# Kernel tuning notes

Measured on AMD Instinct MI355X. Metric: run time of the kernel, lower is better.

The kernel has to match this reference:

```python
import jax, jax.numpy as jnp
import numpy as np

I, H, O = 256, 512, 256  # input_size, hidden_size, output_size
B, S = 4096, 50


def _lstm_cell(x_t, h, c, Wih, Whh, bih, bhh):
    # torch gate order: i, f, g, o
    gates = x_t @ Wih.T + h @ Whh.T + bih + bhh  # [B, 4H]
    i, f, g, o = jnp.split(gates, 4, axis=-1)
    i = jax.nn.sigmoid(i)
    f = jax.nn.sigmoid(f)
    g = jnp.tanh(g)
    o = jax.nn.sigmoid(o)
    c_new = f * c + i * g
    h_new = o * jnp.tanh(c_new)
    return h_new, c_new


def setup_inputs() -> dict:
    key = jax.random.key(0)
    ks = jax.random.split(key, 12)
    s_i = 1.0 / np.sqrt(H)  # torch LSTM/Linear init scale
    u = lambda k, shape: jax.random.uniform(k, shape, jnp.float32, -s_i, s_i)
    return {
        "x": jax.random.normal(ks[0], (B, S, I), jnp.float32),
        "enc_Wih": u(ks[1], (4 * H, I)),
        "enc_Whh": u(ks[2], (4 * H, H)),
        "enc_bih": u(ks[3], (4 * H,)),
        "enc_bhh": u(ks[4], (4 * H,)),
        "dec_Wih": u(ks[5], (4 * H, I)),
        "dec_Whh": u(ks[6], (4 * H, H)),
        "dec_bih": u(ks[7], (4 * H,)),
        "dec_bhh": u(ks[8], (4 * H,)),
        "fc_W": u(ks[9], (O, H)),
        "fc_b": u(ks[10], (O,)),
        "target_seq_length": 20,
    }


def reference(x, enc_Wih, enc_Whh, enc_bih, enc_bhh,
              dec_Wih, dec_Whh, dec_bih, dec_bhh,
              fc_W, fc_b, target_seq_length):
    batch = x.shape[0]
    h0 = jnp.zeros((batch, H), x.dtype)
    c0 = jnp.zeros((batch, H), x.dtype)

    # ---- encoder: scan over time ----
    def enc_step(carry, x_t):
        h, c = carry
        h, c = _lstm_cell(x_t, h, c, enc_Wih, enc_Whh, enc_bih, enc_bhh)
        return (h, c), None

    (h, c), _ = jax.lax.scan(enc_step, (h0, c0), jnp.swapaxes(x, 0, 1))

    dec_in0 = jnp.zeros((batch, I), x.dtype)

    def dec_step(carry, _):
        h, c, inp = carry
        h, c = _lstm_cell(inp, h, c, dec_Wih, dec_Whh, dec_bih, dec_bhh)
        out = h @ fc_W.T + fc_b  # [B, O]
        return (h, c, out), out

    _, outs = jax.lax.scan(dec_step, (h, c, dec_in0), None,
                           length=target_seq_length)
    return jnp.swapaxes(outs, 0, 1)  # [B, T, O]
```

## Files before the change

kernel.cpp:

```cpp
#include <hip/hip_runtime.h>

#define I_SZ 256
#define H_SZ 512
#define O_SZ 256
#define B_SZ 4096
#define S_SZ 50
#define T_SZ 20
#define G4H  2048
#define BH   ((size_t)B_SZ * H_SZ)
#define NB   512
#define NSTEP (S_SZ + T_SZ)

#define PAD 72

typedef _Float16 half8 __attribute__((ext_vector_type(8)));
typedef float f32x4 __attribute__((ext_vector_type(4)));

__device__ __forceinline__ float sigm(float x) {
    return 1.0f / (1.0f + __expf(-x));
}
__device__ __forceinline__ float tanh_fast(float x) {
    float e = __expf(2.0f * x);
    return 1.0f - 2.0f / (e + 1.0f);
}

#define GLDS(gp, lp, aux) __builtin_amdgcn_global_load_lds(                 \
    (const __attribute__((address_space(1))) void*)(gp),                    \
    (__attribute__((address_space(3))) void*)(lp), 16, 0, (aux))

__global__ void k_zeroN(unsigned* p, int n) {
    int i = blockIdx.x * blockDim.x + threadIdx.x;
    if (i < n) p[i] = 0u;
}

__global__ void k_cvt(const float* __restrict__ src, _Float16* __restrict__ dst, int n) {
    int i = blockIdx.x * blockDim.x + threadIdx.x;
    if (i < n) dst[i] = (_Float16)src[i];
}

__global__ void k_bias_combine(const float* __restrict__ a, const float* __restrict__ b,
                               float* __restrict__ dst, int n) {
    int i = blockIdx.x * blockDim.x + threadIdx.x;
    if (i < n) dst[i] = a[i] + b[i];
}

__global__ __launch_bounds__(256) void k_cvt_x(const float* __restrict__ x,
                                               _Float16* __restrict__ xT) {
    size_t idx = ((size_t)blockIdx.x * 256 + threadIdx.x) * 8;
    int i = (int)(idx & 255);
    int s = (int)((idx >> 8) % S_SZ);
    size_t b = idx / (256 * S_SZ);
    float4 v0 = *(const float4*)(x + idx);
    float4 v1 = *(const float4*)(x + idx + 4);
    half8 hv;
    hv[0] = (_Float16)v0.x; hv[1] = (_Float16)v0.y;
    hv[2] = (_Float16)v0.z; hv[3] = (_Float16)v0.w;
    hv[4] = (_Float16)v1.x; hv[5] = (_Float16)v1.y;
    hv[6] = (_Float16)v1.z; hv[7] = (_Float16)v1.w;
    *(half8*)(xT + (((size_t)s * B_SZ + b) * I_SZ + i)) = hv;
}

__global__ void k_wenc(const float* __restrict__ eWih, const float* __restrict__ eWhh,
                       _Float16* __restrict__ Wenc) {
    int idx = blockIdx.x * blockDim.x + threadIdx.x;
    int r = idx / 768, col = idx % 768;
    float v = (col < 256) ? eWih[(size_t)r * 256 + col] : eWhh[(size_t)r * 512 + col - 256];
    Wenc[idx] = (_Float16)v;
}

__global__ __launch_bounds__(256) void k_wd(
    const float* __restrict__ dWhh, const float* __restrict__ dWih,
    const float* __restrict__ fcW, _Float16* __restrict__ Wd)
{
    __shared__ float sA[8][256];
    const int tid = threadIdx.x;
    const int r0 = blockIdx.x * 8;
    {
        int linear = tid * 8;
        int row = linear >> 8, col = linear & 255;
        const float4* p = (const float4*)(dWih + (size_t)(r0 + row) * 256 + col);
        float4 v0 = p[0], v1 = p[1];
        *(float4*)&sA[row][col]     = v0;
        *(float4*)&sA[row][col + 4] = v1;
    }
    __syncthreads();
    float acc[8][2] = {};
    const int k = tid;
    for (int i = 0; i < 256; ++i) {
        float w0 = fcW[(size_t)i * 512 + k];
        float w1 = fcW[(size_t)i * 512 + k + 256];
        #pragma unroll
        for (int rr = 0; rr < 8; ++rr) {
            float a = sA[rr][i];
            acc[rr][0] += a * w0;
            acc[rr][1] += a * w1;
        }
    }
    #pragma unroll
    for (int rr = 0; rr < 8; ++rr) {
        size_t base = (size_t)(r0 + rr) * 512;
        Wd[base + k]       = (_Float16)(dWhh[base + k]       + acc[rr][0]);
        Wd[base + k + 256] = (_Float16)(dWhh[base + k + 256] + acc[rr][1]);
    }
}

__global__ __launch_bounds__(256) void k_bd(
    const float* __restrict__ dWih, const float* __restrict__ fcb,
    const float* __restrict__ db, float* __restrict__ bd)
{
    __shared__ float sf[256];
    const int tid = threadIdx.x;
    sf[tid] = fcb[tid];
    __syncthreads();
    int r = blockIdx.x * 256 + tid;
    float acc = db[r];
    const float* row = dWih + (size_t)r * 256;
    for (int o = 0; o < 256; o += 4) {
        float4 v = *(const float4*)(row + o);
        acc += v.x * sf[o] + v.y * sf[o + 1] + v.z * sf[o + 2] + v.w * sf[o + 3];
    }
    bd[r] = acc;
}

__global__ __launch_bounds__(256, 2) void k_lstm_all(
    const _Float16* __restrict__ xT,
    const _Float16* __restrict__ Wenc,
    const _Float16* __restrict__ dWhh_h,
    const _Float16* __restrict__ Wd,
    const float* __restrict__ eb, const float* __restrict__ db,
    const float* __restrict__ bd,
    _Float16* __restrict__ h0buf, _Float16* __restrict__ h1buf,
    _Float16* __restrict__ hseq,
    unsigned* __restrict__ bar)
{
    __shared__ _Float16 lds[2][2][128 * 64];

    const int tid = threadIdx.x;
    const int xcd = blockIdx.x & 7, slot = blockIdx.x >> 3;
    const int mb = xcd * 4 + (slot >> 4);
    const int jb = slot & 15;
    const int m0 = mb * 128, j0 = jb * 32;
    unsigned* grp = bar + mb * 16;

    const int wv = tid >> 6, lane = tid & 63, lrow = lane & 15, lk8 = (lane >> 4) * 8;
    const int wm = wv >> 1, wn = wv & 1;

    const int colb  = (lane & 7) * 16;
    const int scolh = (colb ^ (((lane >> 3) & 7) << 4)) >> 1;
    int rowq[4], growq[4];
    #pragma unroll
    for (int q = 0; q < 4; ++q) {
        int r = q * 32 + wv * 8 + (lane >> 3);
        rowq[q] = r;
        growq[q] = ((r >> 4) & 3) * H_SZ + j0 + (r >> 6) * 16 + (r & 15);
    }

    float ebj[4], dbj[4], bdj[4];
    #pragma unroll
    for (int nf = 0; nf < 4; ++nf) {
        int col = nf * H_SZ + j0 + wn * 16 + lrow;
        ebj[nf] = eb[col]; dbj[nf] = db[col]; bdj[nf] = bd[col];
    }

    float creg[4][4];

    for (int step = 0; step < NSTEP; ++step) {
        const _Float16* xsrc; const _Float16* hin; const _Float16* W;
        _Float16* hout; int wstride, nx, niter;
        if (step < S_SZ) {
            xsrc = xT + (size_t)step * B_SZ * I_SZ;
            W = Wenc; wstride = 768; nx = 4;
            niter = (step == 0) ? 4 : 12;
            hin  = (step == 0) ? nullptr : ((step & 1) ? h0buf : h1buf);
            hout = (step == S_SZ - 1) ? hseq : ((step & 1) ? h1buf : h0buf);
        } else {
            int t = step - S_SZ;
            xsrc = nullptr; nx = 0; niter = 8; wstride = 512;
            W = (t == 0) ? dWhh_h : Wd;
            hin  = hseq + (size_t)t * BH;
            hout = hseq + (size_t)(t + 1) * BH;
        }

        auto wait_group = [&]() {
            if (tid == 0) {
                unsigned target = (unsigned)step * 16u;
                while (__hip_atomic_load(grp, __ATOMIC_RELAXED, __HIP_MEMORY_SCOPE_AGENT) < target)
                    __builtin_amdgcn_s_sleep(1);
            }
            __syncthreads();
        };

        auto stage = [&](int buf, int it) {
            const int koffW = it * 64;
            #pragma unroll
            for (int q = 0; q < 4; ++q) {
                const _Float16* gb = W + (size_t)growq[q] * wstride + koffW + scolh;
                GLDS(gb, &lds[buf][1][(q * 256 + wv * 64) * 8], 0);
            }
            if (it < nx) {
                #pragma unroll
                for (int q = 0; q < 4; ++q) {
                    const _Float16* ga = xsrc + (size_t)(m0 + rowq[q]) * I_SZ + it * 64 + scolh;
                    GLDS(ga, &lds[buf][0][(q * 256 + wv * 64) * 8], 0);
                }
            } else {
                #pragma unroll
                for (int q = 0; q < 4; ++q) {
                    const _Float16* ga = hin + (size_t)(m0 + rowq[q]) * H_SZ + (it - nx) * 64 + scolh;
                    GLDS(ga, &lds[buf][0][(q * 256 + wv * 64) * 8], 17);
                }
            }
        };

        f32x4 acc[4][4];
        #pragma unroll
        for (int mf = 0; mf < 4; ++mf)
            #pragma unroll
            for (int nf = 0; nf < 4; ++nf) {
                f32x4 z = {0.f, 0.f, 0.f, 0.f};
                acc[mf][nf] = z;
            }

        auto compute = [&](int buf) {
            #pragma unroll
            for (int kc = 0; kc < 2; ++kc) {
                const int cb = (kc * 32 + lk8) * 2;
                const int sc = (cb ^ ((lrow & 7) << 4)) >> 1;
                half8 a[4], b[4];
                #pragma unroll
                for (int mf = 0; mf < 4; ++mf)
                    a[mf] = *(const half8*)&lds[buf][0][(wm * 64 + mf * 16 + lrow) * 64 + sc];
                #pragma unroll
                for (int nf = 0; nf < 4; ++nf)
                    b[nf] = *(const half8*)&lds[buf][1][(wn * 64 + nf * 16 + lrow) * 64 + sc];
                #pragma unroll
                for (int mf = 0; mf < 4; ++mf)
                    #pragma unroll
                    for (int nf = 0; nf < 4; ++nf)
                        acc[mf][nf] = __builtin_amdgcn_mfma_f32_16x16x32_f16(a[mf], b[nf], acc[mf][nf], 0, 0, 0);
            }
        };

        if (step > 0 && nx == 0) wait_group();
        stage(0, 0);
        __syncthreads();
        int buf = 0;
        for (int it = 0; it < niter; ++it) {
            if (it + 1 < niter) {
                if (step > 0 && it + 1 == nx) wait_group();
                stage(buf ^ 1, it + 1);
            }
            compute(buf);
            __syncthreads();
            buf ^= 1;
        }

        float bj[4];
        #pragma unroll
        for (int nf = 0; nf < 4; ++nf)
            bj[nf] = (step < S_SZ) ? ebj[nf] : ((step == S_SZ) ? dbj[nf] : bdj[nf]);

        _Float16* hsm = &lds[0][0][0];
        const int lc = wn * 16 + lrow;
        #pragma unroll
        for (int mf = 0; mf < 4; ++mf)
            #pragma unroll
            for (int r = 0; r < 4; ++r) {
                int lr = wm * 64 + mf * 16 + (lane >> 4) * 4 + r;
                float gi = acc[mf][0][r] + bj[0];
                float gf = acc[mf][1][r] + bj[1];
                float gg = acc[mf][2][r] + bj[2];
                float go = acc[mf][3][r] + bj[3];
                float cold = (step == 0) ? 0.0f : creg[mf][r];
                float cn = sigm(gf) * cold + sigm(gi) * tanh_fast(gg);
                creg[mf][r] = cn;
                hsm[lr * 32 + lc] = (_Float16)(sigm(go) * tanh_fast(cn));
            }
        __syncthreads();
        {
            int row = tid >> 1, seg = tid & 1;
            const unsigned long long* src =
                (const unsigned long long*)&hsm[row * 32 + seg * 16];
            unsigned long long v0 = src[0], v1 = src[1], v2 = src[2], v3 = src[3];
            unsigned long long* dst =
                (unsigned long long*)(hout + (size_t)(m0 + row) * H_SZ + j0 + seg * 16);
            __hip_atomic_store(dst + 0, v0, __ATOMIC_RELAXED, __HIP_MEMORY_SCOPE_AGENT);
            __hip_atomic_store(dst + 1, v1, __ATOMIC_RELAXED, __HIP_MEMORY_SCOPE_AGENT);
            __hip_atomic_store(dst + 2, v2, __ATOMIC_RELAXED, __HIP_MEMORY_SCOPE_AGENT);
            __hip_atomic_store(dst + 3, v3, __ATOMIC_RELAXED, __HIP_MEMORY_SCOPE_AGENT);
        }

        if (step != NSTEP - 1) {
            __syncthreads();
            if (tid == 0)
                __hip_atomic_fetch_add(grp, 1u, __ATOMIC_RELAXED, __HIP_MEMORY_SCOPE_AGENT);
        }
    }
}

__global__ __launch_bounds__(256) void k_fc(
    const _Float16* __restrict__ hseq1,
    const _Float16* __restrict__ W,
    const float* __restrict__ bias,
    float* __restrict__ out)
{
    __shared__ _Float16 Asm[128][PAD];
    __shared__ _Float16 Bsm[128][PAD];

    const int tid = threadIdx.x;
    const int m0 = blockIdx.x * 128;
    const int t  = blockIdx.y;
    const int n0 = blockIdx.z * 128;
    const int wv = tid >> 6, lane = tid & 63, lrow = lane & 15, lk = (lane >> 4) * 8;
    const int wm = wv >> 1, wn = wv & 1;

    f32x4 acc[4][4] = {};

    const int srow = tid >> 3, skc = (tid & 7) * 8;
    const _Float16* A = hseq1 + (size_t)t * BH;

    for (int k0 = 0; k0 < H_SZ; k0 += 64) {
        __syncthreads();
        #pragma unroll
        for (int q = 0; q < 4; ++q) {
            int r = srow + q * 32;
            *(half8*)&Asm[r][skc] = *(const half8*)(A + (size_t)(m0 + r) * H_SZ + k0 + skc);
        }
        #pragma unroll
        for (int q = 0; q < 4; ++q) {
            int rr = srow + q * 32;
            *(half8*)&Bsm[rr][skc] = *(const half8*)(W + (size_t)(n0 + rr) * H_SZ + k0 + skc);
        }
        __syncthreads();
        #pragma unroll
        for (int kc = 0; kc < 64; kc += 32) {
            half8 a[4], b[4];
            #pragma unroll
            for (int mf = 0; mf < 4; ++mf) a[mf] = *(const half8*)&Asm[wm * 64 + mf * 16 + lrow][kc + lk];
            #pragma unroll
            for (int nf = 0; nf < 4; ++nf) b[nf] = *(const half8*)&Bsm[wn * 64 + nf * 16 + lrow][kc + lk];
            #pragma unroll
            for (int mf = 0; mf < 4; ++mf)
                #pragma unroll
                for (int nf = 0; nf < 4; ++nf)
                    acc[mf][nf] = __builtin_amdgcn_mfma_f32_16x16x32_f16(a[mf], b[nf], acc[mf][nf], 0, 0, 0);
        }
    }

    #pragma unroll
    for (int mf = 0; mf < 4; ++mf)
        #pragma unroll
        for (int nf = 0; nf < 4; ++nf) {
            int o = n0 + wn * 64 + nf * 16 + lrow;
            float bv = bias[o];
            #pragma unroll
            for (int r = 0; r < 4; ++r) {
                int m = m0 + wm * 64 + mf * 16 + (lane >> 4) * 4 + r;
                out[(size_t)m * (T_SZ * O_SZ) + (size_t)t * O_SZ + o] = acc[mf][nf][r] + bv;
            }
        }
}

extern "C" void kernel_launch(void* const* d_in, const int* in_sizes, int n_in,
                              void* d_out, int out_size, void* d_ws, size_t ws_size,
                              hipStream_t stream) {
    (void)in_sizes; (void)n_in; (void)out_size; (void)ws_size;

    const float* x    = (const float*)d_in[0];
    const float* eWih = (const float*)d_in[1];
    const float* eWhh = (const float*)d_in[2];
    const float* ebih = (const float*)d_in[3];
    const float* ebhh = (const float*)d_in[4];
    const float* dWih = (const float*)d_in[5];
    const float* dWhh = (const float*)d_in[6];
    const float* dbih = (const float*)d_in[7];
    const float* dbhh = (const float*)d_in[8];
    const float* fcW  = (const float*)d_in[9];
    const float* fcb  = (const float*)d_in[10];
    float* out = (float*)d_out;
    char* ws = (char*)d_ws;

    size_t off = 0;
    auto alloc = [&](size_t bytes) -> void* {
        void* p = ws + off;
        off += (bytes + 255) & ~(size_t)255;
        return p;
    };
    _Float16* xT     = (_Float16*)alloc((size_t)S_SZ * B_SZ * I_SZ * 2);
    _Float16* Wenc   = (_Float16*)alloc((size_t)G4H * (I_SZ + H_SZ) * 2);
    _Float16* dWhh_h = (_Float16*)alloc((size_t)G4H * H_SZ * 2);
    _Float16* Wd     = (_Float16*)alloc((size_t)G4H * H_SZ * 2);
    _Float16* fcW_h  = (_Float16*)alloc((size_t)O_SZ * H_SZ * 2);
    float*    eb     = (float*)alloc(G4H * 4);
    float*    db     = (float*)alloc(G4H * 4);
    float*    bd     = (float*)alloc(G4H * 4);
    _Float16* h0     = (_Float16*)alloc(BH * 2);
    _Float16* h1     = (_Float16*)alloc(BH * 2);
    _Float16* hseq   = (_Float16*)alloc((size_t)(T_SZ + 1) * BH * 2);
    unsigned* bar    = (unsigned*)alloc(32 * 16 * 4);

    const int nWhh = G4H * H_SZ;
    const int nFc  = O_SZ * H_SZ;
    const size_t nX = (size_t)B_SZ * S_SZ * I_SZ;

    k_zeroN<<<2, 256, 0, stream>>>(bar, 32 * 16);
    k_cvt_x<<<(int)(nX / 8 / 256), 256, 0, stream>>>(x, xT);
    k_wenc<<<(G4H * 768) / 256, 256, 0, stream>>>(eWih, eWhh, Wenc);
    k_cvt<<<(nWhh + 255) / 256, 256, 0, stream>>>(dWhh, dWhh_h, nWhh);
    k_cvt<<<(nFc + 255) / 256, 256, 0, stream>>>(fcW, fcW_h, nFc);
    k_bias_combine<<<8, 256, 0, stream>>>(ebih, ebhh, eb, G4H);
    k_bias_combine<<<8, 256, 0, stream>>>(dbih, dbhh, db, G4H);
    k_wd<<<256, 256, 0, stream>>>(dWhh, dWih, fcW, Wd);
    k_bd<<<8, 256, 0, stream>>>(dWih, fcb, db, bd);

    k_lstm_all<<<NB, 256, 0, stream>>>(xT, Wenc, dWhh_h, Wd, eb, db, bd,
                                       h0, h1, hseq, bar);

    k_fc<<<dim3(B_SZ / 128, T_SZ, O_SZ / 128), 256, 0, stream>>>(
        hseq + BH, fcW_h, fcb, out);
}
```

Baseline: 1.512 ms.

## Use explicit vmcnt waits and raw barriers in LSTM pipeline; pad h staging

Replaces __syncthreads in the double-buffered K loop with explicit s_waitcnt vmcnt plus s_barrier, so the next tile's global_load_lds stays in flight while the current tile is computed. Pads the LDS h staging buffer to a 36-element stride to reduce bank conflicts. Rewrites the h writeback so each thread stores coalesced 8-byte chunks across rows. The hand-written vmcnt counts assume a fixed number of outstanding loads and add ordering risk if the compiler emits other memory ops.

```diff
diff --git a/kernel.cpp b/kernel.cpp
--- a/kernel.cpp
+++ b/kernel.cpp
@@ -12,6 +12,7 @@
 #define NSTEP (S_SZ + T_SZ)
 
 #define PAD 72
+#define PAD_H 36
 
 typedef _Float16 half8 __attribute__((ext_vector_type(8)));
 typedef float f32x4 __attribute__((ext_vector_type(4)));
@@ -27,6 +28,8 @@
 #define GLDS(gp, lp, aux) __builtin_amdgcn_global_load_lds(                 \
     (const __attribute__((address_space(1))) void*)(gp),                    \
     (__attribute__((address_space(3))) void*)(lp), 16, 0, (aux))
+
+#define MEMFENCE asm volatile("" ::: "memory")
 
 __global__ void k_zeroN(unsigned* p, int n) {
     int i = blockIdx.x * blockDim.x + threadIdx.x;
@@ -182,12 +185,14 @@
         }
 
         auto wait_group = [&]() {
+            MEMFENCE;
             if (tid == 0) {
                 unsigned target = (unsigned)step * 16u;
                 while (__hip_atomic_load(grp, __ATOMIC_RELAXED, __HIP_MEMORY_SCOPE_AGENT) < target)
                     __builtin_amdgcn_s_sleep(1);
             }
-            __syncthreads();
+            __builtin_amdgcn_s_barrier();
+            MEMFENCE;
         };
 
         auto stage = [&](int buf, int it) {
@@ -243,15 +248,21 @@
 
         if (step > 0 && nx == 0) wait_group();
         stage(0, 0);
-        __syncthreads();
         int buf = 0;
         for (int it = 0; it < niter; ++it) {
             if (it + 1 < niter) {
-                if (step > 0 && it + 1 == nx) wait_group();
+                if (step > 0 && nx > 0 && it + 1 == nx) wait_group();
                 stage(buf ^ 1, it + 1);
-            }
+                asm volatile("s_waitcnt vmcnt(8)" ::: "memory");
+            } else {
+                asm volatile("s_waitcnt vmcnt(0)" ::: "memory");
+            }
+            __builtin_amdgcn_s_barrier();
+            MEMFENCE;
             compute(buf);
-            __syncthreads();
+            MEMFENCE;
+            __builtin_amdgcn_s_barrier();
+            MEMFENCE;
             buf ^= 1;
         }
 
@@ -274,20 +285,19 @@
                 float cold = (step == 0) ? 0.0f : creg[mf][r];
                 float cn = sigm(gf) * cold + sigm(gi) * tanh_fast(gg);
                 creg[mf][r] = cn;
-                hsm[lr * 32 + lc] = (_Float16)(sigm(go) * tanh_fast(cn));
+                hsm[lr * PAD_H + lc] = (_Float16)(sigm(go) * tanh_fast(cn));
             }
         __syncthreads();
         {
-            int row = tid >> 1, seg = tid & 1;
-            const unsigned long long* src =
-                (const unsigned long long*)&hsm[row * 32 + seg * 16];
-            unsigned long long v0 = src[0], v1 = src[1], v2 = src[2], v3 = src[3];
-            unsigned long long* dst =
-                (unsigned long long*)(hout + (size_t)(m0 + row) * H_SZ + j0 + seg * 16);
-            __hip_atomic_store(dst + 0, v0, __ATOMIC_RELAXED, __HIP_MEMORY_SCOPE_AGENT);
-            __hip_atomic_store(dst + 1, v1, __ATOMIC_RELAXED, __HIP_MEMORY_SCOPE_AGENT);
-            __hip_atomic_store(dst + 2, v2, __ATOMIC_RELAXED, __HIP_MEMORY_SCOPE_AGENT);
-            __hip_atomic_store(dst + 3, v3, __ATOMIC_RELAXED, __HIP_MEMORY_SCOPE_AGENT);
+            int rr = tid >> 3, k = tid & 7;
+            #pragma unroll
+            for (int q = 0; q < 4; ++q) {
+                int r = rr + q * 32;
+                unsigned long long v = *(const unsigned long long*)&hsm[r * PAD_H + k * 4];
+                unsigned long long* dst =
+                    (unsigned long long*)(hout + (size_t)(m0 + r) * H_SZ + j0) + k;
+                __hip_atomic_store(dst, v, __ATOMIC_RELAXED, __HIP_MEMORY_SCOPE_AGENT);
+            }
         }
 
         if (step != NSTEP - 1) {
```

New measurement: 1.331 ms. 12.0% less time.
